# Performance work log

Measured on AMD Instinct MI355X. Metric: run time of the kernel, lower is better.

The kernel has to match this reference:

```python
import jax, jax.numpy as jnp
import numpy as np

EMBED = 1024
HEADS = 16


def setup_inputs() -> dict:
    key = jax.random.key(0)
    ks = jax.random.split(key, 5)
    N, L, E = 4, 4096, EMBED
    s = 0.02  # weight init scale
    return {
        "x": jax.random.normal(ks[0], (N, L, E), dtype=jnp.float32),
        "Wq": jax.random.normal(ks[1], (E, E), dtype=jnp.float32) * s,
        "Wk": jax.random.normal(ks[2], (E, E), dtype=jnp.float32) * s,
        "Wv": jax.random.normal(ks[3], (E, E), dtype=jnp.float32) * s,
        "Wo": jax.random.normal(ks[4], (E, E), dtype=jnp.float32) * s,
        "bo": jnp.zeros((E,), dtype=jnp.float32),
    }


def reference(x, Wq, Wk, Wv, Wo, bo):
    # Faithful translation of the torch module, INCLUDING its permute/einsum quirk:
    # after permute, q/k/v are (N, H, L, D) and einsum 'nqhd,nkhd->nqk' contracts
    # over length (h) and head_dim (d), yielding an (N, H, H) energy tensor.
    N, L, E = x.shape
    H = HEADS
    D = E // H

    def proj(W):
        # torch nn.Linear: y = x @ W.T ; then view + permute(0,2,1,3) -> (N,H,L,D)
        y = jnp.einsum('nle,fe->nlf', x, W)
        return y.reshape(N, L, H, D).transpose(0, 2, 1, 3)

    q = proj(Wq)  # (N, H, L, D)
    k = proj(Wk)
    v = proj(Wv)

    energy = jnp.einsum('nqhd,nkhd->nqk', q, k)  # (N, H, H): contracts L and D
    attention = jax.nn.softmax(energy / jnp.sqrt(jnp.float32(E)), axis=2)
    # 'nqk,nvhd->nqhd': k summed in attention only, v summed in values only
    out = jnp.einsum('nqk,nvhd->nqhd', attention, v)  # (N, H, L, D)
    out = out.reshape(N, L, H * D)  # layout-scrambling reshape, as in torch
    return jnp.einsum('nle,fe->nlf', out, Wo) + bo
```

## Files before the change

### kernel.cpp

```cpp
#include <hip/hip_runtime.h>
#include <hip/hip_bf16.h>

#define L_SEQ 4096
#define EMB   1024

__global__ void k_wvsum(const float* __restrict__ Wv, float* __restrict__ Wvsum) {
    int g = blockIdx.x * blockDim.x + threadIdx.x;
    int d = g >> 10;
    int e = g & 1023;
    float s = 0.f;
#pragma unroll
    for (int h = 0; h < 16; ++h)
        s += Wv[(h * 64 + d) * 1024 + e];
    Wvsum[g] = s;
}

__global__ __launch_bounds__(256) void k_vsum(const float* __restrict__ x,
                                              const float* __restrict__ Wvsum,
                                              float* __restrict__ vsum) {
    __shared__ float4 As[16][33];
    __shared__ float4 Bs[16][65];

    const int t  = threadIdx.x;
    const int c0 = t & 15;
    const int r0 = t >> 4;
    const int R0 = blockIdx.x * 32;

    float acc[2][4] = {{0.f,0.f,0.f,0.f},{0.f,0.f,0.f,0.f}};

    for (int e0 = 0; e0 < 1024; e0 += 64) {
#pragma unroll
        for (int u = 0; u < 2; ++u)
            As[c0][r0 + 16*u] = *reinterpret_cast<const float4*>(
                &x[(size_t)(R0 + r0 + 16*u) * 1024 + e0 + c0 * 4]);
#pragma unroll
        for (int u = 0; u < 4; ++u)
            Bs[c0][r0 + 16*u] = *reinterpret_cast<const float4*>(
                &Wvsum[(r0 + 16*u) * 1024 + e0 + c0 * 4]);
        __syncthreads();

#pragma unroll
        for (int kk = 0; kk < 16; ++kk) {
            float4 a0 = As[kk][r0];
            float4 a1 = As[kk][r0 + 16];
            float4 b[4];
#pragma unroll
            for (int j = 0; j < 4; ++j) b[j] = Bs[kk][c0 + 16*j];
#pragma unroll
            for (int j = 0; j < 4; ++j) {
                acc[0][j] = fmaf(a0.x, b[j].x, acc[0][j]);
                acc[0][j] = fmaf(a0.y, b[j].y, acc[0][j]);
                acc[0][j] = fmaf(a0.z, b[j].z, acc[0][j]);
                acc[0][j] = fmaf(a0.w, b[j].w, acc[0][j]);
                acc[1][j] = fmaf(a1.x, b[j].x, acc[1][j]);
                acc[1][j] = fmaf(a1.y, b[j].y, acc[1][j]);
                acc[1][j] = fmaf(a1.z, b[j].z, acc[1][j]);
                acc[1][j] = fmaf(a1.w, b[j].w, acc[1][j]);
            }
        }
        __syncthreads();
    }

#pragma unroll
    for (int i = 0; i < 2; ++i)
#pragma unroll
        for (int j = 0; j < 4; ++j)
            vsum[(size_t)(R0 + r0 + 16*i) * 64 + c0 + 16*j] = acc[i][j];
}

__global__ __launch_bounds__(256) void k_out(const float* __restrict__ Z,
                                             const float* __restrict__ Wo,
                                             const float* __restrict__ bo,
                                             float* __restrict__ out) {
    __shared__ float4 As[16][33];
    __shared__ float4 Bs[16][65];

    const int t  = threadIdx.x;
    const int c0 = t & 15;
    const int r0 = t >> 4;
    const int rt = blockIdx.x & 31;
    const int ct = blockIdx.x >> 5;
    const int ZR0 = rt * 32;
    const int F0  = ct * 64;

    float acc[2][4] = {{0.f,0.f,0.f,0.f},{0.f,0.f,0.f,0.f}};

    for (int e0 = 0; e0 < 1024; e0 += 64) {
#pragma unroll
        for (int u = 0; u < 2; ++u)
            As[c0][r0 + 16*u] = *reinterpret_cast<const float4*>(
                &Z[(size_t)(ZR0 + r0 + 16*u) * 1024 + e0 + c0 * 4]);
#pragma unroll
        for (int u = 0; u < 4; ++u)
            Bs[c0][r0 + 16*u] = *reinterpret_cast<const float4*>(
                &Wo[(size_t)(F0 + r0 + 16*u) * 1024 + e0 + c0 * 4]);
        __syncthreads();

#pragma unroll
        for (int kk = 0; kk < 16; ++kk) {
            float4 a0 = As[kk][r0];
            float4 a1 = As[kk][r0 + 16];
            float4 b[4];
#pragma unroll
            for (int j = 0; j < 4; ++j) b[j] = Bs[kk][c0 + 16*j];
#pragma unroll
            for (int j = 0; j < 4; ++j) {
                acc[0][j] = fmaf(a0.x, b[j].x, acc[0][j]);
                acc[0][j] = fmaf(a0.y, b[j].y, acc[0][j]);
                acc[0][j] = fmaf(a0.z, b[j].z, acc[0][j]);
                acc[0][j] = fmaf(a0.w, b[j].w, acc[0][j]);
                acc[1][j] = fmaf(a1.x, b[j].x, acc[1][j]);
                acc[1][j] = fmaf(a1.y, b[j].y, acc[1][j]);
                acc[1][j] = fmaf(a1.z, b[j].z, acc[1][j]);
                acc[1][j] = fmaf(a1.w, b[j].w, acc[1][j]);
            }
        }
        __syncthreads();
    }

#pragma unroll
    for (int i = 0; i < 2; ++i) {
        const int zr = ZR0 + r0 + 16*i;
        const int n  = zr >> 8;
        const int m  = zr & 255;
        const size_t base_n = (size_t)n * L_SEQ * EMB;
#pragma unroll
        for (int j = 0; j < 4; ++j) {
            const int f = F0 + c0 + 16*j;
            const float val = acc[i][j] + bo[f];
#pragma unroll
            for (int q = 0; q < 16; ++q)
                out[base_n + (size_t)(q * 256 + m) * EMB + f] = val;
        }
    }
}

extern "C" void kernel_launch(void* const* d_in, const int* in_sizes, int n_in,
                              void* d_out, int out_size, void* d_ws, size_t ws_size,
                              hipStream_t stream) {
    const float* x  = (const float*)d_in[0];
    const float* Wv = (const float*)d_in[3];
    const float* Wo = (const float*)d_in[4];
    const float* bo = (const float*)d_in[5];
    float* out = (float*)d_out;

    float* Wvsum = (float*)d_ws;
    float* vsum  = Wvsum + 64 * 1024;

    k_wvsum<<<256, 256, 0, stream>>>(Wv, Wvsum);
    k_vsum <<<512, 256, 0, stream>>>(x, Wvsum, vsum);
    k_out  <<<512, 256, 0, stream>>>(vsum, Wo, bo, out);
}
```

Baseline: 213.0 us.

## Rewrite vsum and output GEMMs with split-bf16 MFMA and vectorized nontemporal stores

Replaces the FP32 FMA tiled GEMMs with MFMA 16x16x32 bf16 kernels. Each FP32 operand is split into bf16 high and low parts and three products are summed to keep near-FP32 accuracy. The Wv head-sum is packed into an MFMA-friendly bf16 layout, and the output kernel stages results through shared memory so it can issue float4 nontemporal stores of the 16x replicated output. The aim is to move compute onto matrix cores and speed up the write-bound output. The cost is extra conversion arithmetic per tile and a small loss of precision.

```diff
diff --git a/kernel.cpp b/kernel.cpp
--- a/kernel.cpp
+++ b/kernel.cpp
@@ -1,137 +1,222 @@
 #include <hip/hip_runtime.h>
 #include <hip/hip_bf16.h>
 
-#define L_SEQ 4096
-#define EMB   1024
-
-__global__ void k_wvsum(const float* __restrict__ Wv, float* __restrict__ Wvsum) {
-    int g = blockIdx.x * blockDim.x + threadIdx.x;
-    int d = g >> 10;
-    int e = g & 1023;
-    float s = 0.f;
-#pragma unroll
-    for (int h = 0; h < 16; ++h)
-        s += Wv[(h * 64 + d) * 1024 + e];
-    Wvsum[g] = s;
-}
-
-__global__ __launch_bounds__(256) void k_vsum(const float* __restrict__ x,
-                                              const float* __restrict__ Wvsum,
-                                              float* __restrict__ vsum) {
-    __shared__ float4 As[16][33];
-    __shared__ float4 Bs[16][65];
-
-    const int t  = threadIdx.x;
-    const int c0 = t & 15;
-    const int r0 = t >> 4;
-    const int R0 = blockIdx.x * 32;
-
-    float acc[2][4] = {{0.f,0.f,0.f,0.f},{0.f,0.f,0.f,0.f}};
-
-    for (int e0 = 0; e0 < 1024; e0 += 64) {
-#pragma unroll
-        for (int u = 0; u < 2; ++u)
-            As[c0][r0 + 16*u] = *reinterpret_cast<const float4*>(
-                &x[(size_t)(R0 + r0 + 16*u) * 1024 + e0 + c0 * 4]);
-#pragma unroll
-        for (int u = 0; u < 4; ++u)
-            Bs[c0][r0 + 16*u] = *reinterpret_cast<const float4*>(
-                &Wvsum[(r0 + 16*u) * 1024 + e0 + c0 * 4]);
-        __syncthreads();
-
-#pragma unroll
-        for (int kk = 0; kk < 16; ++kk) {
-            float4 a0 = As[kk][r0];
-            float4 a1 = As[kk][r0 + 16];
-            float4 b[4];
-#pragma unroll
-            for (int j = 0; j < 4; ++j) b[j] = Bs[kk][c0 + 16*j];
+
+typedef unsigned short u16;
+typedef __attribute__((ext_vector_type(8))) short  short8v;
+typedef __attribute__((ext_vector_type(4))) float  f32x4;
+typedef __attribute__((ext_vector_type(4))) u16    ushort4v;
+
+__device__ __forceinline__ u16 f2bf(float f) {
+    unsigned u = __float_as_uint(f);
+    u += 0x7fffu + ((u >> 16) & 1u);
+    return (u16)(u >> 16);
+}
+__device__ __forceinline__ float bf2f(u16 h) {
+    return __uint_as_float(((unsigned)h) << 16);
+}
+__device__ __forceinline__ f32x4 mfma16(short8v a, short8v b, f32x4 c) {
+    return __builtin_amdgcn_mfma_f32_16x16x32_bf16(a, b, c, 0, 0, 0);
+}
+
+__global__ __launch_bounds__(256) void k_pack_b(const float* __restrict__ Wv,
+                                                u16* __restrict__ Bh,
+                                                u16* __restrict__ Bl) {
+    int t  = blockIdx.x * 256 + threadIdx.x;
+    int c  = t >> 7;
+    int e8 = t & 127;
+    int e  = e8 << 3;
+    float ss[8] = {0.f,0.f,0.f,0.f,0.f,0.f,0.f,0.f};
+#pragma unroll
+    for (int h = 0; h < 16; ++h) {
+        const f32x4* p = (const f32x4*)&Wv[(size_t)((h << 6) + c) * 1024 + e];
+        f32x4 a = p[0], b = p[1];
+        ss[0]+=a[0]; ss[1]+=a[1]; ss[2]+=a[2]; ss[3]+=a[3];
+        ss[4]+=b[0]; ss[5]+=b[1]; ss[6]+=b[2]; ss[7]+=b[3];
+    }
+    short8v h8, l8;
+#pragma unroll
+    for (int j = 0; j < 8; ++j) {
+        u16 hh = f2bf(ss[j]);
+        h8[j] = (short)hh;
+        l8[j] = (short)f2bf(ss[j] - bf2f(hh));
+    }
+    ((short8v*)Bh)[e8 * 64 + c] = h8;
+    ((short8v*)Bl)[e8 * 64 + c] = l8;
+}
+
+__global__ __launch_bounds__(256) void k_vsum_mfma(const float* __restrict__ x,
+                                                   const u16* __restrict__ Bh,
+                                                   const u16* __restrict__ Bl,
+                                                   float* __restrict__ Z) {
+    __shared__ __align__(16) u16 Ah[32][136];
+    __shared__ __align__(16) u16 Al[32][136];
+
+    const int t    = threadIdx.x;
+    const int lane = t & 63;
+    const int w    = t >> 6;
+    const int l15  = lane & 15;
+    const int lh   = lane >> 4;
+    const int cb   = w << 4;
+    const int R0   = blockIdx.x << 5;
+
+    const int sr = t >> 3;
+    const int se = (t & 7) << 4;
+
+    const short8v* bh8 = (const short8v*)Bh;
+    const short8v* bl8 = (const short8v*)Bl;
+
+    f32x4 acc0 = {0.f,0.f,0.f,0.f};
+    f32x4 acc1 = {0.f,0.f,0.f,0.f};
+
+    for (int ch = 0; ch < 8; ++ch) {
+        const int e0 = ch << 7;
+#pragma unroll
+        for (int q = 0; q < 4; ++q) {
+            f32x4 v = *(const f32x4*)&x[(size_t)(R0 + sr) * 1024 + e0 + se + (q << 2)];
+            ushort4v h4, l4;
 #pragma unroll
             for (int j = 0; j < 4; ++j) {
-                acc[0][j] = fmaf(a0.x, b[j].x, acc[0][j]);
-                acc[0][j] = fmaf(a0.y, b[j].y, acc[0][j]);
-                acc[0][j] = fmaf(a0.z, b[j].z, acc[0][j]);
-                acc[0][j] = fmaf(a0.w, b[j].w, acc[0][j]);
-                acc[1][j] = fmaf(a1.x, b[j].x, acc[1][j]);
-                acc[1][j] = fmaf(a1.y, b[j].y, acc[1][j]);
-                acc[1][j] = fmaf(a1.z, b[j].z, acc[1][j]);
-                acc[1][j] = fmaf(a1.w, b[j].w, acc[1][j]);
+                u16 hh = f2bf(v[j]);
+                h4[j] = hh;
+                l4[j] = f2bf(v[j] - bf2f(hh));
             }
-        }
-        __syncthreads();
-    }
-
-#pragma unroll
-    for (int i = 0; i < 2; ++i)
-#pragma unroll
-        for (int j = 0; j < 4; ++j)
-            vsum[(size_t)(R0 + r0 + 16*i) * 64 + c0 + 16*j] = acc[i][j];
-}
-
-__global__ __launch_bounds__(256) void k_out(const float* __restrict__ Z,
-                                             const float* __restrict__ Wo,
-                                             const float* __restrict__ bo,
-                                             float* __restrict__ out) {
-    __shared__ float4 As[16][33];
-    __shared__ float4 Bs[16][65];
-
-    const int t  = threadIdx.x;
-    const int c0 = t & 15;
-    const int r0 = t >> 4;
-    const int rt = blockIdx.x & 31;
-    const int ct = blockIdx.x >> 5;
-    const int ZR0 = rt * 32;
-    const int F0  = ct * 64;
-
-    float acc[2][4] = {{0.f,0.f,0.f,0.f},{0.f,0.f,0.f,0.f}};
-
-    for (int e0 = 0; e0 < 1024; e0 += 64) {
-#pragma unroll
-        for (int u = 0; u < 2; ++u)
-            As[c0][r0 + 16*u] = *reinterpret_cast<const float4*>(
-                &Z[(size_t)(ZR0 + r0 + 16*u) * 1024 + e0 + c0 * 4]);
-#pragma unroll
-        for (int u = 0; u < 4; ++u)
-            Bs[c0][r0 + 16*u] = *reinterpret_cast<const float4*>(
-                &Wo[(size_t)(F0 + r0 + 16*u) * 1024 + e0 + c0 * 4]);
-        __syncthreads();
-
-#pragma unroll
-        for (int kk = 0; kk < 16; ++kk) {
-            float4 a0 = As[kk][r0];
-            float4 a1 = As[kk][r0 + 16];
-            float4 b[4];
-#pragma unroll
-            for (int j = 0; j < 4; ++j) b[j] = Bs[kk][c0 + 16*j];
-#pragma unroll
-            for (int j = 0; j < 4; ++j) {
-                acc[0][j] = fmaf(a0.x, b[j].x, acc[0][j]);
-                acc[0][j] = fmaf(a0.y, b[j].y, acc[0][j]);
-                acc[0][j] = fmaf(a0.z, b[j].z, acc[0][j]);
-                acc[0][j] = fmaf(a0.w, b[j].w, acc[0][j]);
-                acc[1][j] = fmaf(a1.x, b[j].x, acc[1][j]);
-                acc[1][j] = fmaf(a1.y, b[j].y, acc[1][j]);
-                acc[1][j] = fmaf(a1.z, b[j].z, acc[1][j]);
-                acc[1][j] = fmaf(a1.w, b[j].w, acc[1][j]);
+            *(ushort4v*)&Ah[sr][se + (q << 2)] = h4;
+            *(ushort4v*)&Al[sr][se + (q << 2)] = l4;
+        }
+        __syncthreads();
+#pragma unroll
+        for (int ktl = 0; ktl < 4; ++ktl) {
+            const int koff = (ktl << 5) + (lh << 3);
+            short8v ah0 = *(const short8v*)&Ah[l15][koff];
+            short8v al0 = *(const short8v*)&Al[l15][koff];
+            short8v ah1 = *(const short8v*)&Ah[16 + l15][koff];
+            short8v al1 = *(const short8v*)&Al[16 + l15][koff];
+            const int ktg  = (ch << 2) + ktl;
+            const int bidx = ((ktg << 2) + lh) * 64 + cb + l15;
+            short8v bhf = bh8[bidx];
+            short8v blf = bl8[bidx];
+            acc0 = mfma16(ah0, bhf, acc0);
+            acc0 = mfma16(ah0, blf, acc0);
+            acc0 = mfma16(al0, bhf, acc0);
+            acc1 = mfma16(ah1, bhf, acc1);
+            acc1 = mfma16(ah1, blf, acc1);
+            acc1 = mfma16(al1, bhf, acc1);
+        }
+        __syncthreads();
+    }
+    const int zrbase = blockIdx.x << 1;
+#pragma unroll
+    for (int reg = 0; reg < 4; ++reg) {
+        int v15 = (lh << 2) + reg;
+        Z[(size_t)zrbase       * 1024 + v15 * 64 + cb + l15] = acc0[reg];
+        Z[(size_t)(zrbase + 1) * 1024 + v15 * 64 + cb + l15] = acc1[reg];
+    }
+}
+
+__global__ __launch_bounds__(256) void k_out_mfma(const float* __restrict__ Z,
+                                                  const float* __restrict__ Wo,
+                                                  const float* __restrict__ bo,
+                                                  float* __restrict__ out) {
+    __shared__ __align__(16) unsigned char smem[2 * 64 * 136 * 2];
+    u16 (*Zh)[136] = (u16(*)[136])smem;
+    u16 (*Zl)[136] = (u16(*)[136])(smem + 64 * 136 * 2);
+
+    const int t    = threadIdx.x;
+    const int lane = t & 63;
+    const int w    = t >> 6;
+    const int l15  = lane & 15;
+    const int lh   = lane >> 4;
+    const int zr0  = (blockIdx.x & 15) << 6;
+    const int f0   = (blockIdx.x >> 4) << 6;
+    const int fb   = f0 + (w << 4);
+
+    const int sr = t >> 4;
+    const int se = (t & 15) << 3;
+
+    const f32x4* wrow = (const f32x4*)&Wo[(size_t)(fb + l15) * 1024];
+
+    f32x4 acc0 = {0.f,0.f,0.f,0.f};
+    f32x4 acc1 = {0.f,0.f,0.f,0.f};
+    f32x4 acc2 = {0.f,0.f,0.f,0.f};
+    f32x4 acc3 = {0.f,0.f,0.f,0.f};
+
+    for (int ch = 0; ch < 8; ++ch) {
+        const int e0 = ch << 7;
+#pragma unroll
+        for (int p = 0; p < 4; ++p) {
+            int r = (p << 4) + sr;
+#pragma unroll
+            for (int qq = 0; qq < 2; ++qq) {
+                f32x4 v = *(const f32x4*)&Z[(size_t)(zr0 + r) * 1024 + e0 + se + (qq << 2)];
+                ushort4v h4, l4;
+#pragma unroll
+                for (int j = 0; j < 4; ++j) {
+                    u16 hh = f2bf(v[j]);
+                    h4[j] = hh;
+                    l4[j] = f2bf(v[j] - bf2f(hh));
+                }
+                *(ushort4v*)&Zh[r][se + (qq << 2)] = h4;
+                *(ushort4v*)&Zl[r][se + (qq << 2)] = l4;
             }
         }
         __syncthreads();
-    }
-
-#pragma unroll
-    for (int i = 0; i < 2; ++i) {
-        const int zr = ZR0 + r0 + 16*i;
-        const int n  = zr >> 8;
-        const int m  = zr & 255;
-        const size_t base_n = (size_t)n * L_SEQ * EMB;
-#pragma unroll
-        for (int j = 0; j < 4; ++j) {
-            const int f = F0 + c0 + 16*j;
-            const float val = acc[i][j] + bo[f];
-#pragma unroll
-            for (int q = 0; q < 16; ++q)
-                out[base_n + (size_t)(q * 256 + m) * EMB + f] = val;
-        }
+#pragma unroll
+        for (int ktl = 0; ktl < 4; ++ktl) {
+            const int koff = (ktl << 5) + (lh << 3);
+            const int widx = (e0 + koff) >> 2;
+            f32x4 w0 = wrow[widx], w1 = wrow[widx + 1];
+            short8v bhf, blf;
+            {
+                float wf[8] = {w0[0], w0[1], w0[2], w0[3], w1[0], w1[1], w1[2], w1[3]};
+#pragma unroll
+                for (int j = 0; j < 8; ++j) {
+                    u16 hh = f2bf(wf[j]);
+                    bhf[j] = (short)hh;
+                    blf[j] = (short)f2bf(wf[j] - bf2f(hh));
+                }
+            }
+            short8v ah, al;
+            ah = *(const short8v*)&Zh[l15][koff];
+            al = *(const short8v*)&Zl[l15][koff];
+            acc0 = mfma16(ah, bhf, acc0); acc0 = mfma16(ah, blf, acc0); acc0 = mfma16(al, bhf, acc0);
+            ah = *(const short8v*)&Zh[16 + l15][koff];
+            al = *(const short8v*)&Zl[16 + l15][koff];
+            acc1 = mfma16(ah, bhf, acc1); acc1 = mfma16(ah, blf, acc1); acc1 = mfma16(al, bhf, acc1);
+            ah = *(const short8v*)&Zh[32 + l15][koff];
+            al = *(const short8v*)&Zl[32 + l15][koff];
+            acc2 = mfma16(ah, bhf, acc2); acc2 = mfma16(ah, blf, acc2); acc2 = mfma16(al, bhf, acc2);
+            ah = *(const short8v*)&Zh[48 + l15][koff];
+            al = *(const short8v*)&Zl[48 + l15][koff];
+            acc3 = mfma16(ah, bhf, acc3); acc3 = mfma16(ah, blf, acc3); acc3 = mfma16(al, bhf, acc3);
+        }
+        __syncthreads();
+    }
+
+    float (*Ut)[68] = (float(*)[68])smem;
+    const float bov = bo[fb + l15];
+#pragma unroll
+    for (int reg = 0; reg < 4; ++reg) {
+        int rl = (lh << 2) + reg;
+        int cl = (w << 4) + l15;
+        Ut[rl     ][cl] = acc0[reg] + bov;
+        Ut[16 + rl][cl] = acc1[reg] + bov;
+        Ut[32 + rl][cl] = acc2[reg] + bov;
+        Ut[48 + rl][cl] = acc3[reg] + bov;
+    }
+    __syncthreads();
+
+    const int fq = t & 15, rr = t >> 4;
+#pragma unroll
+    for (int p = 0; p < 4; ++p) {
+        int r = (p << 4) + rr;
+        f32x4 val = *(const f32x4*)&Ut[r][fq << 2];
+        int zr = zr0 + r;
+        float* ob = out + ((size_t)(zr >> 8) << 22) + ((size_t)(zr & 255) << 10)
+                        + f0 + (fq << 2);
+#pragma unroll
+        for (int q = 0; q < 16; ++q)
+            __builtin_nontemporal_store(val, (f32x4*)(ob + ((size_t)q << 18)));
     }
 }
 
@@ -144,10 +229,11 @@
     const float* bo = (const float*)d_in[5];
     float* out = (float*)d_out;
 
-    float* Wvsum = (float*)d_ws;
-    float* vsum  = Wvsum + 64 * 1024;
-
-    k_wvsum<<<256, 256, 0, stream>>>(Wv, Wvsum);
-    k_vsum <<<512, 256, 0, stream>>>(x, Wvsum, vsum);
-    k_out  <<<512, 256, 0, stream>>>(vsum, Wo, bo, out);
-}
+    u16*   Bh = (u16*)d_ws;
+    u16*   Bl = Bh + 64 * 1024;
+    float* Z  = (float*)(Bl + 64 * 1024);
+
+    k_pack_b   <<<32,  256, 0, stream>>>(Wv, Bh, Bl);
+    k_vsum_mfma<<<512, 256, 0, stream>>>(x, Bh, Bl, Z);
+    k_out_mfma <<<256, 256, 0, stream>>>(Z, Wo, bo, out);
+}
```

After: 189.5 us. 11.0% less time.

## Rewrite both GEMMs with split-bf16 MFMA and a separate broadcast store kernel

Applied to the files above, without the earlier changes.

Replaces the scalar FP32 shared-memory GEMMs with bf16 MFMA 16x16x32 instructions. Each fp32 operand is split into high and low bf16 parts and three MFMAs per tile recover close to fp32 accuracy. K is split across waves and the partial sums are reduced through LDS. Wv summation and Wo packing are fused into one prep kernel, and scratch lives in the tail of the output buffer. The 16x replicated output write moves to a dedicated broadcast kernel using nontemporal stores. The changes trade extra conversion work and lower precision for matrix-core throughput and better store coalescing.

```diff
diff --git a/kernel.cpp b/kernel.cpp
--- a/kernel.cpp
+++ b/kernel.cpp
@@ -1,138 +1,182 @@
 #include <hip/hip_runtime.h>
 #include <hip/hip_bf16.h>
 
-#define L_SEQ 4096
-#define EMB   1024
-
-__global__ void k_wvsum(const float* __restrict__ Wv, float* __restrict__ Wvsum) {
-    int g = blockIdx.x * blockDim.x + threadIdx.x;
-    int d = g >> 10;
-    int e = g & 1023;
-    float s = 0.f;
-#pragma unroll
-    for (int h = 0; h < 16; ++h)
-        s += Wv[(h * 64 + d) * 1024 + e];
-    Wvsum[g] = s;
-}
-
-__global__ __launch_bounds__(256) void k_vsum(const float* __restrict__ x,
-                                              const float* __restrict__ Wvsum,
-                                              float* __restrict__ vsum) {
-    __shared__ float4 As[16][33];
-    __shared__ float4 Bs[16][65];
-
-    const int t  = threadIdx.x;
-    const int c0 = t & 15;
-    const int r0 = t >> 4;
-    const int R0 = blockIdx.x * 32;
-
-    float acc[2][4] = {{0.f,0.f,0.f,0.f},{0.f,0.f,0.f,0.f}};
-
-    for (int e0 = 0; e0 < 1024; e0 += 64) {
-#pragma unroll
-        for (int u = 0; u < 2; ++u)
-            As[c0][r0 + 16*u] = *reinterpret_cast<const float4*>(
-                &x[(size_t)(R0 + r0 + 16*u) * 1024 + e0 + c0 * 4]);
-#pragma unroll
-        for (int u = 0; u < 4; ++u)
-            Bs[c0][r0 + 16*u] = *reinterpret_cast<const float4*>(
-                &Wvsum[(r0 + 16*u) * 1024 + e0 + c0 * 4]);
-        __syncthreads();
-
-#pragma unroll
-        for (int kk = 0; kk < 16; ++kk) {
-            float4 a0 = As[kk][r0];
-            float4 a1 = As[kk][r0 + 16];
-            float4 b[4];
-#pragma unroll
-            for (int j = 0; j < 4; ++j) b[j] = Bs[kk][c0 + 16*j];
-#pragma unroll
-            for (int j = 0; j < 4; ++j) {
-                acc[0][j] = fmaf(a0.x, b[j].x, acc[0][j]);
-                acc[0][j] = fmaf(a0.y, b[j].y, acc[0][j]);
-                acc[0][j] = fmaf(a0.z, b[j].z, acc[0][j]);
-                acc[0][j] = fmaf(a0.w, b[j].w, acc[0][j]);
-                acc[1][j] = fmaf(a1.x, b[j].x, acc[1][j]);
-                acc[1][j] = fmaf(a1.y, b[j].y, acc[1][j]);
-                acc[1][j] = fmaf(a1.z, b[j].z, acc[1][j]);
-                acc[1][j] = fmaf(a1.w, b[j].w, acc[1][j]);
-            }
-        }
-        __syncthreads();
-    }
-
-#pragma unroll
-    for (int i = 0; i < 2; ++i)
-#pragma unroll
-        for (int j = 0; j < 4; ++j)
-            vsum[(size_t)(R0 + r0 + 16*i) * 64 + c0 + 16*j] = acc[i][j];
-}
-
-__global__ __launch_bounds__(256) void k_out(const float* __restrict__ Z,
-                                             const float* __restrict__ Wo,
-                                             const float* __restrict__ bo,
-                                             float* __restrict__ out) {
-    __shared__ float4 As[16][33];
-    __shared__ float4 Bs[16][65];
-
-    const int t  = threadIdx.x;
-    const int c0 = t & 15;
-    const int r0 = t >> 4;
-    const int rt = blockIdx.x & 31;
-    const int ct = blockIdx.x >> 5;
-    const int ZR0 = rt * 32;
-    const int F0  = ct * 64;
-
-    float acc[2][4] = {{0.f,0.f,0.f,0.f},{0.f,0.f,0.f,0.f}};
-
-    for (int e0 = 0; e0 < 1024; e0 += 64) {
-#pragma unroll
-        for (int u = 0; u < 2; ++u)
-            As[c0][r0 + 16*u] = *reinterpret_cast<const float4*>(
-                &Z[(size_t)(ZR0 + r0 + 16*u) * 1024 + e0 + c0 * 4]);
-#pragma unroll
-        for (int u = 0; u < 4; ++u)
-            Bs[c0][r0 + 16*u] = *reinterpret_cast<const float4*>(
-                &Wo[(size_t)(F0 + r0 + 16*u) * 1024 + e0 + c0 * 4]);
-        __syncthreads();
-
-#pragma unroll
-        for (int kk = 0; kk < 16; ++kk) {
-            float4 a0 = As[kk][r0];
-            float4 a1 = As[kk][r0 + 16];
-            float4 b[4];
-#pragma unroll
-            for (int j = 0; j < 4; ++j) b[j] = Bs[kk][c0 + 16*j];
-#pragma unroll
-            for (int j = 0; j < 4; ++j) {
-                acc[0][j] = fmaf(a0.x, b[j].x, acc[0][j]);
-                acc[0][j] = fmaf(a0.y, b[j].y, acc[0][j]);
-                acc[0][j] = fmaf(a0.z, b[j].z, acc[0][j]);
-                acc[0][j] = fmaf(a0.w, b[j].w, acc[0][j]);
-                acc[1][j] = fmaf(a1.x, b[j].x, acc[1][j]);
-                acc[1][j] = fmaf(a1.y, b[j].y, acc[1][j]);
-                acc[1][j] = fmaf(a1.z, b[j].z, acc[1][j]);
-                acc[1][j] = fmaf(a1.w, b[j].w, acc[1][j]);
-            }
-        }
-        __syncthreads();
-    }
-
-#pragma unroll
-    for (int i = 0; i < 2; ++i) {
-        const int zr = ZR0 + r0 + 16*i;
-        const int n  = zr >> 8;
-        const int m  = zr & 255;
-        const size_t base_n = (size_t)n * L_SEQ * EMB;
-#pragma unroll
-        for (int j = 0; j < 4; ++j) {
-            const int f = F0 + c0 + 16*j;
-            const float val = acc[i][j] + bo[f];
-#pragma unroll
-            for (int q = 0; q < 16; ++q)
-                out[base_n + (size_t)(q * 256 + m) * EMB + f] = val;
-        }
-    }
+
+typedef unsigned short u16;
+typedef __attribute__((ext_vector_type(8))) short  short8v;
+typedef __attribute__((ext_vector_type(4))) float  f32x4;
+typedef __attribute__((ext_vector_type(4))) u16    ushort4v;
+
+__device__ __forceinline__ u16 f2bf(float f) {
+    unsigned u = __float_as_uint(f);
+    u += 0x7fffu + ((u >> 16) & 1u);
+    return (u16)(u >> 16);
+}
+__device__ __forceinline__ float bf2f(u16 h) {
+    return __uint_as_float(((unsigned)h) << 16);
+}
+__device__ __forceinline__ f32x4 mfma16(short8v a, short8v b, f32x4 c) {
+    return __builtin_amdgcn_mfma_f32_16x16x32_bf16(a, b, c, 0, 0, 0);
+}
+__device__ __forceinline__ void split8(f32x4 v0, f32x4 v1, short8v& h8, short8v& l8) {
+    float wf[8] = {v0[0],v0[1],v0[2],v0[3],v1[0],v1[1],v1[2],v1[3]};
+#pragma unroll
+    for (int j = 0; j < 8; ++j) {
+        u16 hh = f2bf(wf[j]);
+        h8[j] = (short)hh;
+        l8[j] = (short)f2bf(wf[j] - bf2f(hh));
+    }
+}
+
+__global__ __launch_bounds__(256) void k_pack(const float* __restrict__ Wv,
+                                              const float* __restrict__ Wo,
+                                              u16* __restrict__ Bh, u16* __restrict__ Bl,
+                                              u16* __restrict__ Woh, u16* __restrict__ Wol) {
+    const int b = blockIdx.x;
+    if (b < 512) {
+        const int g = b * 256 + threadIdx.x;
+        const f32x4* p = (const f32x4*)(Wo + (size_t)g * 8);
+        short8v h8, l8; split8(p[0], p[1], h8, l8);
+        ((short8v*)Woh)[g] = h8;
+        ((short8v*)Wol)[g] = l8;
+    } else {
+        const int t  = (b - 512) * 256 + threadIdx.x;
+        const int c  = t >> 7;
+        const int e8 = t & 127;
+        f32x4 s0 = {0,0,0,0}, s1 = {0,0,0,0};
+#pragma unroll
+        for (int h = 0; h < 16; ++h) {
+            const f32x4* p = (const f32x4*)&Wv[(size_t)((h << 6) + c) * 1024 + (e8 << 3)];
+            s0 += p[0]; s1 += p[1];
+        }
+        short8v h8, l8; split8(s0, s1, h8, l8);
+        ((short8v*)Bh)[e8 * 64 + c] = h8;
+        ((short8v*)Bl)[e8 * 64 + c] = l8;
+    }
+}
+
+__global__ __launch_bounds__(256, 4) void k_vsum(const float* __restrict__ x,
+                                                 const u16* __restrict__ Bh,
+                                                 const u16* __restrict__ Bl,
+                                                 u16* __restrict__ Zh,
+                                                 u16* __restrict__ Zl) {
+    __shared__ float red[4][64][16];
+    const int t = threadIdx.x, lane = t & 63, w = t >> 6;
+    const int l15 = lane & 15, lh = lane >> 4;
+    const int g = blockIdx.x;
+    const int R0 = g << 4;
+    const int kbase = w << 8;
+    const short8v* bh8 = (const short8v*)Bh;
+    const short8v* bl8 = (const short8v*)Bl;
+
+    f32x4 acc[4] = {{0,0,0,0},{0,0,0,0},{0,0,0,0},{0,0,0,0}};
+
+#pragma unroll 2
+    for (int kt = 0; kt < 8; ++kt) {
+        const int k0 = kbase + (kt << 5);
+        const float* ap = &x[(size_t)(R0 + l15) * 1024 + k0 + (lh << 3)];
+        f32x4 a0 = __builtin_nontemporal_load((const f32x4*)ap);
+        f32x4 a1 = __builtin_nontemporal_load((const f32x4*)(ap + 4));
+        short8v ah, al; split8(a0, a1, ah, al);
+        const int e8 = (k0 >> 3) + lh;
+#pragma unroll
+        for (int cg = 0; cg < 4; ++cg) {
+            short8v bh = bh8[e8 * 64 + (cg << 4) + l15];
+            short8v bl = bl8[e8 * 64 + (cg << 4) + l15];
+            acc[cg] = mfma16(ah, bh, acc[cg]);
+            acc[cg] = mfma16(ah, bl, acc[cg]);
+            acc[cg] = mfma16(al, bh, acc[cg]);
+        }
+    }
+
+#pragma unroll
+    for (int cg = 0; cg < 4; ++cg)
+#pragma unroll
+        for (int reg = 0; reg < 4; ++reg)
+            red[w][lane][(cg << 2) + reg] = acc[cg][reg];
+    __syncthreads();
+
+    ushort4v zh, zl;
+#pragma unroll
+    for (int j = 0; j < 4; ++j) {
+        const int e = (t << 2) + j, v15 = e >> 6, c = e & 63;
+        const int ln = ((v15 >> 2) << 4) | (c & 15);
+        const int slot = ((c >> 4) << 2) | (v15 & 3);
+        float s = red[0][ln][slot] + red[1][ln][slot] + red[2][ln][slot] + red[3][ln][slot];
+        u16 hh = f2bf(s);
+        zh[j] = hh;
+        zl[j] = f2bf(s - bf2f(hh));
+    }
+    *(ushort4v*)&Zh[((size_t)g << 10) + (t << 2)] = zh;
+    *(ushort4v*)&Zl[((size_t)g << 10) + (t << 2)] = zl;
+}
+
+__global__ __launch_bounds__(512, 2) void k_ugemm(const u16* __restrict__ Zh,
+                                                  const u16* __restrict__ Zl,
+                                                  const u16* __restrict__ Woh,
+                                                  const u16* __restrict__ Wol,
+                                                  const float* __restrict__ bo,
+                                                  float* __restrict__ out) {
+    __shared__ float red[8][64][16];
+    const int t = threadIdx.x, lane = t & 63, w = t >> 6;
+    const int l15 = lane & 15, lh = lane >> 4;
+    const int rg = w & 3, kh = w >> 2;
+    const int rt = blockIdx.x & 15, ct = blockIdx.x >> 4;
+    const int rbase = (rt << 6) + (rg << 4), fbase = ct << 6;
+
+    f32x4 acc[4] = {{0,0,0,0},{0,0,0,0},{0,0,0,0},{0,0,0,0}};
+    const size_t arow = (size_t)(rbase + l15) << 10;
+
+#pragma unroll 2
+    for (int kt = 0; kt < 16; ++kt) {
+        const int k0 = (kh << 9) + (kt << 5) + (lh << 3);
+        short8v ah = *(const short8v*)&Zh[arow + k0];
+        short8v al = *(const short8v*)&Zl[arow + k0];
+#pragma unroll
+        for (int cg = 0; cg < 4; ++cg) {
+            const size_t brow = (size_t)(fbase + (cg << 4) + l15) << 10;
+            short8v bh = *(const short8v*)&Woh[brow + k0];
+            short8v bl = *(const short8v*)&Wol[brow + k0];
+            acc[cg] = mfma16(ah, bh, acc[cg]);
+            acc[cg] = mfma16(ah, bl, acc[cg]);
+            acc[cg] = mfma16(al, bh, acc[cg]);
+        }
+    }
+
+#pragma unroll
+    for (int cg = 0; cg < 4; ++cg)
+#pragma unroll
+        for (int reg = 0; reg < 4; ++reg)
+            red[w][lane][(cg << 2) + reg] = acc[cg][reg];
+    __syncthreads();
+
+    const int r = t >> 3, cbase = (t & 7) << 3;
+    const int rg2 = r >> 4, lh2 = (r & 15) >> 2, reg2 = r & 3;
+    const int ur = (rt << 6) + r;
+    const int n = ur >> 8, m = ur & 255;
+    float* ob = out + ((size_t)n << 22) + ((size_t)m << 10) + fbase + cbase;
+#pragma unroll
+    for (int jj = 0; jj < 2; ++jj) {
+        f32x4 o;
+#pragma unroll
+        for (int q = 0; q < 4; ++q) {
+            const int c = cbase + (jj << 2) + q;
+            const int ln = (lh2 << 4) | (c & 15);
+            const int slot = ((c >> 4) << 2) | reg2;
+            o[q] = red[rg2][ln][slot] + red[4 + rg2][ln][slot] + bo[fbase + c];
+        }
+        *(f32x4*)(ob + (jj << 2)) = o;
+    }
+}
+
+__global__ __launch_bounds__(256) void k_bcast(float* __restrict__ out) {
+    const int T = blockIdx.x * 256 + threadIdx.x;
+    const int f4 = T & 255, m = (T >> 8) & 255, n = T >> 16;
+    float* src = out + ((size_t)n << 22) + ((size_t)m << 10) + (f4 << 2);
+    f32x4 v = *(const f32x4*)src;
+#pragma unroll
+    for (int q = 1; q < 16; ++q)
+        __builtin_nontemporal_store(v, (f32x4*)(src + ((size_t)q << 18)));
 }
 
 extern "C" void kernel_launch(void* const* d_in, const int* in_sizes, int n_in,
@@ -144,10 +188,16 @@
     const float* bo = (const float*)d_in[5];
     float* out = (float*)d_out;
 
-    float* Wvsum = (float*)d_ws;
-    float* vsum  = Wvsum + 64 * 1024;
-
-    k_wvsum<<<256, 256, 0, stream>>>(Wv, Wvsum);
-    k_vsum <<<512, 256, 0, stream>>>(x, Wvsum, vsum);
-    k_out  <<<512, 256, 0, stream>>>(vsum, Wo, bo, out);
-}
+    u16* Bh = (u16*)d_ws;
+    u16* Bl = Bh + 64 * 1024;
+
+    u16* Woh = (u16*)(out + (size_t)14 * 1024 * 1024);
+    u16* Wol = Woh + 1024 * 1024;
+    u16* Zh  = Wol + 1024 * 1024;
+    u16* Zl  = Zh  + 1024 * 1024;
+
+    k_pack <<<544,  256, 0, stream>>>(Wv, Wo, Bh, Bl, Woh, Wol);
+    k_vsum <<<1024, 256, 0, stream>>>(x, Bh, Bl, Zh, Zl);
+    k_ugemm<<<256,  512, 0, stream>>>(Zh, Zl, Woh, Wol, bo, out);
+    k_bcast<<<1024, 256, 0, stream>>>(out);
+}
```

Result: faster. 190.5 us (-10.5%).
